# Performance work log

Measured on AMD Instinct MI355X. Metric: run time of the kernel, lower is better.

Reference implementation:

```python
import jax, jax.numpy as jnp
import numpy as np

NUM_HEADS = 12
NUM_GROUPS = 4
LN_EPS = 1e-12
NEG = -10000.0


def _ln(x, g, b):
    m = x.mean(-1, keepdims=True)
    v = ((x - m) ** 2).mean(-1, keepdims=True)
    return (x - m) * jax.lax.rsqrt(v + LN_EPS) * g + b


def _attention(h, ext_mask, Wattn, battn, ln):
    # h: [B,S,H]; ext_mask additive [B,1,1,S]; Wattn [4,H,H] = (q,k,v,o); battn [4,H]; ln [2,H]
    B, S, H = h.shape
    dh = H // NUM_HEADS
    q = (h @ Wattn[0] + battn[0]).reshape(B, S, NUM_HEADS, dh)
    k = (h @ Wattn[1] + battn[1]).reshape(B, S, NUM_HEADS, dh)
    v = (h @ Wattn[2] + battn[2]).reshape(B, S, NUM_HEADS, dh)
    scores = jnp.einsum('bqhd,bkhd->bhqk', q, k) * (1.0 / np.sqrt(dh)) + ext_mask
    p = jax.nn.softmax(scores, axis=-1)
    ctx = jnp.einsum('bhqk,bkhd->bqhd', p, v).reshape(B, S, H)
    # BertSelfOutput: dense + residual + LayerNorm
    return _ln(ctx @ Wattn[3] + battn[3] + h, ln[0], ln[1])


def _ffn(x, Wi, bi, Wo, bo, ln):
    # BertIntermediate (gelu) + BertOutput (dense + residual + LayerNorm)
    return _ln(jax.nn.gelu(x @ Wi + bi, approximate=False) @ Wo + bo + x, ln[0], ln[1])


def _bert_layer(h, ext_mask, Wattn, battn, ln_attn, Wi, bi, Wo, bo, ln_out):
    a = _attention(h, ext_mask, Wattn, battn, ln_attn)
    return _ffn(a, Wi, bi, Wo, bo, ln_out)


def _hier_attention(h, hier_mask, Wattn, battn, ln_attn, Wi, bi, Wo, bo, ln_out):
    # group masks [G,B,S]: 1 where hier_mask == group_id (ids 1..G)
    gids = jnp.arange(1, NUM_GROUPS + 1)
    masks = (hier_mask[None] == gids[:, None, None]).astype(h.dtype)  # [G,B,S]
    ext = (1.0 - masks)[:, :, None, None, :] * NEG                    # [G,B,1,1,S]
    # one full BertLayer per group (vectorized over G instead of batch concat)
    outs = jax.vmap(lambda m: _bert_layer(h, m, Wattn, battn, ln_attn, Wi, bi, Wo, bo, ln_out))(ext)  # [G,B,S,H]
    return jnp.sum(outs * masks[..., None], axis=0)


def reference(hidden_states, attention_mask, main_Wattn, main_battn, main_ln_attn,
              main_Wi, main_bi, main_Wo, main_bo, main_ln_out,
              hier_Wattn, hier_battn, hier_ln_attn, hier_Wi, hier_bi, hier_Wo,
              hier_bo, hier_ln_out, hier_mask):
    attn_out = _attention(hidden_states, attention_mask, main_Wattn, main_battn, main_ln_attn)
    hier_out = _hier_attention(hidden_states, hier_mask, hier_Wattn, hier_battn,
                               hier_ln_attn, hier_Wi, hier_bi, hier_Wo, hier_bo, hier_ln_out)
    combined = attn_out + hier_out
    return _ffn(combined, main_Wi, main_bi, main_Wo, main_bo, main_ln_out)


def setup_inputs() -> dict:
    key = jax.random.key(0)
    ks = jax.random.split(key, 20)
    B, S, H, F = 8, 512, 768, 3072
    W = 0.02  # weight init scale

    def layer_params(k):
        kk = jax.random.split(k, 8)
        return dict(
            Wattn=jax.random.normal(kk[0], (4, H, H), jnp.float32) * W,
            battn=jax.random.normal(kk[1], (4, H), jnp.float32) * W,
            ln_attn=jnp.stack([1.0 + jax.random.normal(kk[2], (H,), jnp.float32) * W,
                               jax.random.normal(kk[3], (H,), jnp.float32) * W]),
            Wi=jax.random.normal(kk[4], (H, F), jnp.float32) * W,
            bi=jax.random.normal(kk[5], (F,), jnp.float32) * W,
            Wo=jax.random.normal(kk[6], (F, H), jnp.float32) * W,
            bo=jax.random.normal(kk[7], (H,), jnp.float32) * W,
            ln_out=jnp.stack([1.0 + jax.random.normal(kk[2], (H,), jnp.float32) * W,
                              jax.random.normal(kk[3], (H,), jnp.float32) * W]),
        )

    main = layer_params(ks[0])
    hier = layer_params(ks[1])
    inp = {
        'hidden_states': jax.random.normal(ks[2], (B, S, H), jnp.float32),
        'attention_mask': jnp.zeros((B, 1, 1, S), jnp.float32),
        'hier_mask': jax.random.randint(ks[3], (B, S), 0, 5).astype(jnp.int64),
    }
    for name, p in (('main', main), ('hier', hier)):
        for k2, v in p.items():
            inp[f'{name}_{k2}'] = v
    return inp
```

## Files before the change

kernel.cpp:

```cpp
#include <hip/hip_runtime.h>
#include <hip/hip_bf16.h>

#define DI __device__ __forceinline__

typedef __attribute__((ext_vector_type(4))) float  f32x4;
typedef __attribute__((ext_vector_type(8))) short  s16x8;
typedef __attribute__((ext_vector_type(4))) short  s16x4;
typedef __attribute__((ext_vector_type(8))) __bf16 bf16x8;

DI short f2bf(float f) {
  union { float f; unsigned u; } v; v.f = f;
  unsigned r = v.u + 0x7fffu + ((v.u >> 16) & 1u);
  return (short)(r >> 16);
}

DI f32x4 mfma16(s16x8 a, s16x8 b, f32x4 c) {
  return __builtin_amdgcn_mfma_f32_16x16x32_bf16(
      __builtin_bit_cast(bf16x8, a), __builtin_bit_cast(bf16x8, b), c, 0, 0, 0);
}

typedef const __attribute__((address_space(1))) unsigned* gas_p;
typedef __attribute__((address_space(3))) unsigned* las_p;
DI void gload16(const void* g, void* l) {
  __builtin_amdgcn_global_load_lds((gas_p)g, (las_p)l, 16, 0, 0);
}

__global__ __launch_bounds__(256) void cast_bf16(const float* __restrict__ x,
                                                 short* __restrict__ y) {
  const int i = (blockIdx.x * 256 + threadIdx.x) * 4;
  const float4 t = *(const float4*)&x[i];
  s16x4 o;
  o[0] = f2bf(t.x); o[1] = f2bf(t.y); o[2] = f2bf(t.z); o[3] = f2bf(t.w);
  *(s16x4*)&y[i] = o;
}

struct TJob { const float* src; short* dst; int K, N, tile0; };
struct TJobs { TJob j[12]; };

__global__ __launch_bounds__(256) void transpose_w(TJobs jobs) {
  __shared__ float T[32][33];
  const int t = blockIdx.x;
  int ji = 0;
#pragma unroll
  for (int i = 1; i < 12; ++i) if (jobs.j[i].tile0 <= t) ji = i;
  const float* src = jobs.j[ji].src;
  short* dst = jobs.j[ji].dst;
  const int K = jobs.j[ji].K, N = jobs.j[ji].N;
  const int lt = t - jobs.j[ji].tile0;
  const int tn = N >> 5;
  const int n0 = (lt % tn) << 5, k0 = (lt / tn) << 5;
  const int tid = threadIdx.x;
#pragma unroll
  for (int i = 0; i < 4; ++i) {
    const int c = i * 256 + tid, r = c >> 5, cc = c & 31;
    T[cc][r] = src[(long long)(k0 + r) * N + n0 + cc];
  }
  __syncthreads();
#pragma unroll
  for (int i = 0; i < 4; ++i) {
    const int c = i * 256 + tid, r = c >> 5, cc = c & 31;
    dst[(long long)(n0 + r) * K + k0 + cc] = f2bf(T[r][cc]);
  }
}

__global__ __launch_bounds__(256) void transpose_v(const short* __restrict__ QKV,
                                                   short* __restrict__ Vt) {
  __shared__ short T[64][72];
  const int bh = blockIdx.y;
  const int b = bh / 12, hh = bh % 12;
  const int s0 = blockIdx.x * 64;
  const int tid = threadIdx.x;
#pragma unroll
  for (int i = 0; i < 2; ++i) {
    const int c = i * 256 + tid;
    const int s = c >> 3, d = (c & 7) * 8;
    s16x8 v = *(const s16x8*)&QKV[(long long)(b * 512 + s0 + s) * 2304 + 1536 + hh * 64 + d];
    *(s16x8*)&T[s][d] = v;
  }
  __syncthreads();
#pragma unroll
  for (int i = 0; i < 2; ++i) {
    const int c = i * 256 + tid;
    const int d = c >> 3, s = (c & 7) * 8;
    s16x8 v;
#pragma unroll
    for (int j = 0; j < 8; ++j) v[j] = T[s + j][d];
    *(s16x8*)&Vt[(long long)bh * 32768 + (long long)d * 512 + s0 + s] = v;
  }
}

template<int BM, int BN, int WM, int WN, int EPI>
__global__ __launch_bounds__(256) void gemm_bt(
    const short* __restrict__ A, int lda, long long sA,
    const short* __restrict__ B, int ldb, long long sB,
    void* __restrict__ Cv, int ldc,
    long long cOuter, int cInner, int cStride,
    const float* __restrict__ bias,
    int K, int nSplit) {
  constexpr int BK = 32;
  constexpr int WNW = BN / WN;
  constexpr int MFR = WM / 16, NFR = WN / 16;
  constexpr int ACH = BM * 4;
  constexpr int BCH = BN * 4;

  __shared__ short As[2][BM * BK];
  __shared__ short Bs[2][BN * BK];

  const int z = blockIdx.z;
  const int zb = z / nSplit, zs = z - zb * nSplit;
  const short* Ab = A + (long long)zb * sA + (long long)zs * K;
  const short* Bb = B + (long long)zb * sB + (long long)zs * K;
  const long long cOff = (long long)(z / cInner) * cOuter + (long long)(z % cInner) * cStride;

  const int bm = blockIdx.x * BM;
  const int bn = blockIdx.y * BN;
  const int tid = threadIdx.x;
  const int wave = tid >> 6, lane = tid & 63;
  const int wm = (wave / WNW) * WM;
  const int wn = (wave % WNW) * WN;
  const int l16 = lane & 15, lk = lane >> 4;

  f32x4 acc[MFR][NFR] = {};

  auto stage = [&](int buf, int kt) {
#pragma unroll
    for (int i = 0; i < ACH / 256; ++i) {
      const int c = i * 256 + tid;
      gload16(Ab + (long long)(bm + (c >> 2)) * lda + kt + (c & 3) * 8,
              &As[buf][(i * 256 + wave * 64) * 8]);
    }
#pragma unroll
    for (int i = 0; i < BCH / 256; ++i) {
      const int c = i * 256 + tid;
      gload16(Bb + (long long)(bn + (c >> 2)) * ldb + kt + (c & 3) * 8,
              &Bs[buf][(i * 256 + wave * 64) * 8]);
    }
  };

  stage(0, 0);
  __syncthreads();
  int cur = 0;
  for (int kt = 0; kt < K; kt += BK) {
    if (kt + BK < K) stage(cur ^ 1, kt + BK);
    s16x8 af[MFR], bfr[NFR];
#pragma unroll
    for (int mi = 0; mi < MFR; ++mi)
      af[mi] = *(const s16x8*)&As[cur][(wm + mi * 16 + l16) * BK + lk * 8];
#pragma unroll
    for (int ni = 0; ni < NFR; ++ni)
      bfr[ni] = *(const s16x8*)&Bs[cur][(wn + ni * 16 + l16) * BK + lk * 8];
#pragma unroll
    for (int mi = 0; mi < MFR; ++mi)
#pragma unroll
      for (int ni = 0; ni < NFR; ++ni)
        acc[mi][ni] = mfma16(bfr[ni], af[mi], acc[mi][ni]);
    __syncthreads();
    cur ^= 1;
  }

#pragma unroll
  for (int mi = 0; mi < MFR; ++mi) {
    const int row = bm + wm + mi * 16 + l16;
#pragma unroll
    for (int ni = 0; ni < NFR; ++ni) {
      const int col = bn + wn + ni * 16 + lk * 4;
      const long long idx = cOff + (long long)row * ldc + col;
      f32x4 bv = {};
      if (EPI != 2 && bias) bv = *(const f32x4*)&bias[col];
      f32x4 v = acc[mi][ni] + bv;
      if constexpr (EPI == 0) {
        s16x4 o;
#pragma unroll
        for (int r = 0; r < 4; ++r) o[r] = f2bf(v[r]);
        *(s16x4*)&((short*)Cv)[idx] = o;
      } else if constexpr (EPI == 1) {
        s16x4 o;
#pragma unroll
        for (int r = 0; r < 4; ++r) {
          const float g = 0.5f * v[r] * (1.f + erff(v[r] * 0.70710678118654752f));
          o[r] = f2bf(g);
        }
        *(s16x4*)&((short*)Cv)[idx] = o;
      } else {
        *(f32x4*)&((float*)Cv)[idx] = v;
      }
    }
  }
}

template<int HIER>
__global__ __launch_bounds__(256) void attn_scores(
    const short* __restrict__ QKV,
    const float* __restrict__ amask,
    const int* __restrict__ hmask,
    short* __restrict__ P) {
  __shared__ short Qs[32 * 64];
  __shared__ short Ks[256 * 64];
  __shared__ float red[32 * 4];
  __shared__ int   hm[512];

  const int bh = blockIdx.y;
  const int b = bh / 12, hh = bh % 12;
  const int q0 = blockIdx.x * 32;
  const int tid = threadIdx.x;
  const int wave = tid >> 6, lane = tid & 63;
  const int l16 = lane & 15, lk = lane >> 4;
  const long long rowbase = (long long)(b * 512) * 2304 + hh * 64;

  {
    const int c = tid;
    gload16(QKV + rowbase + (long long)(q0 + (c >> 3)) * 2304 + (c & 7) * 8,
            &Qs[wave * 64 * 8]);
  }
  if constexpr (HIER) {
    for (int i = tid; i < 512; i += 256) hm[i] = hmask[b * 512 + i];
  }

  f32x4 acc[2][8] = {};
#pragma unroll
  for (int kc = 0; kc < 2; ++kc) {
    if (kc) __syncthreads();
#pragma unroll
    for (int i = 0; i < 8; ++i) {
      const int c = i * 256 + tid;
      gload16(QKV + rowbase + 768 + (long long)(kc * 256 + (c >> 3)) * 2304 + (c & 7) * 8,
              &Ks[(i * 256 + wave * 64) * 8]);
    }
    __syncthreads();
#pragma unroll
    for (int ks = 0; ks < 2; ++ks) {
      s16x8 af[2], bfr[4];
#pragma unroll
      for (int mi = 0; mi < 2; ++mi)
        af[mi] = *(const s16x8*)&Qs[(mi * 16 + l16) * 64 + ks * 32 + lk * 8];
#pragma unroll
      for (int ni = 0; ni < 4; ++ni)
        bfr[ni] = *(const s16x8*)&Ks[(wave * 64 + ni * 16 + l16) * 64 + ks * 32 + lk * 8];
#pragma unroll
      for (int mi = 0; mi < 2; ++mi)
#pragma unroll
        for (int ni = 0; ni < 4; ++ni)
          acc[mi][kc * 4 + ni] = mfma16(af[mi], bfr[ni], acc[mi][kc * 4 + ni]);
    }
  }

  int gq[2][4];
  if constexpr (HIER) {
#pragma unroll
    for (int mi = 0; mi < 2; ++mi)
#pragma unroll
      for (int r = 0; r < 4; ++r)
        gq[mi][r] = hm[q0 + mi * 16 + lk * 4 + r];
  }
  int hk[8]; float am[8];
#pragma unroll
  for (int nig = 0; nig < 8; ++nig) {
    const int col = (nig >> 2) * 256 + wave * 64 + (nig & 3) * 16 + l16;
    if constexpr (HIER) hk[nig] = hm[col];
    else                am[nig] = amask[b * 512 + col];
  }
#pragma unroll
  for (int mi = 0; mi < 2; ++mi)
#pragma unroll
    for (int nig = 0; nig < 8; ++nig)
#pragma unroll
      for (int r = 0; r < 4; ++r) {
        float v = acc[mi][nig][r] * 0.125f;
        if constexpr (HIER) v += (hk[nig] == gq[mi][r]) ? 0.f : -10000.f;
        else                v += am[nig];
        acc[mi][nig][r] = v;
      }

  float mx[2][4];
#pragma unroll
  for (int mi = 0; mi < 2; ++mi)
#pragma unroll
    for (int r = 0; r < 4; ++r) {
      float m = acc[mi][0][r];
#pragma unroll
      for (int nig = 1; nig < 8; ++nig) m = fmaxf(m, acc[mi][nig][r]);
#pragma unroll
      for (int d = 1; d < 16; d <<= 1) m = fmaxf(m, __shfl_xor(m, d));
      mx[mi][r] = m;
      red[(mi * 16 + lk * 4 + r) * 4 + wave] = m;
    }
  __syncthreads();
#pragma unroll
  for (int mi = 0; mi < 2; ++mi)
#pragma unroll
    for (int r = 0; r < 4; ++r) {
      const int q = mi * 16 + lk * 4 + r;
      mx[mi][r] = fmaxf(fmaxf(red[q * 4], red[q * 4 + 1]),
                        fmaxf(red[q * 4 + 2], red[q * 4 + 3]));
    }
  __syncthreads();

  float sm[2][4];
#pragma unroll
  for (int mi = 0; mi < 2; ++mi)
#pragma unroll
    for (int r = 0; r < 4; ++r) {
      float s = 0.f;
#pragma unroll
      for (int nig = 0; nig < 8; ++nig) {
        const float e = __expf(acc[mi][nig][r] - mx[mi][r]);
        acc[mi][nig][r] = e;
        s += e;
      }
#pragma unroll
      for (int d = 1; d < 16; d <<= 1) s += __shfl_xor(s, d);
      sm[mi][r] = s;
      red[(mi * 16 + lk * 4 + r) * 4 + wave] = s;
    }
  __syncthreads();
#pragma unroll
  for (int mi = 0; mi < 2; ++mi)
#pragma unroll
    for (int r = 0; r < 4; ++r) {
      const int q = mi * 16 + lk * 4 + r;
      sm[mi][r] = 1.f / (red[q * 4] + red[q * 4 + 1] + red[q * 4 + 2] + red[q * 4 + 3]);
    }

  const long long Pbase = (long long)bh * 512 * 512;
#pragma unroll
  for (int mi = 0; mi < 2; ++mi)
#pragma unroll
    for (int nig = 0; nig < 8; ++nig) {
      const int col = (nig >> 2) * 256 + wave * 64 + (nig & 3) * 16 + l16;
#pragma unroll
      for (int r = 0; r < 4; ++r) {
        const int q = mi * 16 + lk * 4 + r;
        P[Pbase + (long long)(q0 + q) * 512 + col] = f2bf(acc[mi][nig][r] * sm[mi][r]);
      }
    }
}

template<int NS, int MODE>
__global__ __launch_bounds__(256) void ln_red(
    const float* __restrict__ part, const float* __restrict__ bias,
    const float* __restrict__ res, const float* __restrict__ ln,
    float* __restrict__ outf, short* __restrict__ outb,
    const int* __restrict__ hmask) {
  constexpr long long SP = 4096LL * 768;
  const int row = blockIdx.x * 4 + (threadIdx.x >> 6);
  const int lane = threadIdx.x & 63;
  const long long rb = (long long)row * 768;
  float v[12];
  float s = 0.f;
#pragma unroll
  for (int i = 0; i < 3; ++i) {
    const int c4 = lane + (i << 6);
    float4 t = ((const float4*)(res + rb))[c4];
    const float4 bv = ((const float4*)bias)[c4];
    t.x += bv.x; t.y += bv.y; t.z += bv.z; t.w += bv.w;
#pragma unroll
    for (int ss = 0; ss < NS; ++ss) {
      const float4 p = ((const float4*)(part + ss * SP + rb))[c4];
      t.x += p.x; t.y += p.y; t.z += p.z; t.w += p.w;
    }
    v[i * 4 + 0] = t.x; v[i * 4 + 1] = t.y; v[i * 4 + 2] = t.z; v[i * 4 + 3] = t.w;
    s += t.x + t.y + t.z + t.w;
  }
#pragma unroll
  for (int d = 1; d < 64; d <<= 1) s += __shfl_xor(s, d);
  const float mean = s * (1.f / 768.f);
  float vs = 0.f;
#pragma unroll
  for (int i = 0; i < 12; ++i) { const float dv = v[i] - mean; vs += dv * dv; }
#pragma unroll
  for (int d = 1; d < 64; d <<= 1) vs += __shfl_xor(vs, d);
  const float rstd = rsqrtf(vs * (1.f / 768.f) + 1e-12f);
  int keep = 1;
  if constexpr (MODE == 2) keep = (hmask[row] != 0);
#pragma unroll
  for (int i = 0; i < 3; ++i) {
    const int c4 = lane + (i << 6);
    const float4 g = ((const float4*)ln)[c4];
    const float4 be = ((const float4*)(ln + 768))[c4];
    const float gg[4] = {g.x, g.y, g.z, g.w}, bb[4] = {be.x, be.y, be.z, be.w};
    float resv[4];
#pragma unroll
    for (int j = 0; j < 4; ++j) {
      float yv = (v[i * 4 + j] - mean) * rstd * gg[j] + bb[j];
      if constexpr (MODE == 2) {
        const float a = outf[rb + c4 * 4 + j];
        yv = a + (keep ? yv : 0.f);
      }
      resv[j] = yv;
    }
    float4 of; of.x = resv[0]; of.y = resv[1]; of.z = resv[2]; of.w = resv[3];
    ((float4*)(outf + rb))[c4] = of;
    if constexpr (MODE >= 1) {
      s16x4 ob;
#pragma unroll
      for (int j = 0; j < 4; ++j) ob[j] = f2bf(resv[j]);
      *(s16x4*)&outb[rb + c4 * 4] = ob;
    }
  }
}

extern "C" void kernel_launch(void* const* d_in, const int* in_sizes, int n_in,
                              void* d_out, int out_size, void* d_ws, size_t ws_size,
                              hipStream_t stream) {
  (void)in_sizes; (void)n_in; (void)out_size; (void)ws_size;
  const float* h      = (const float*)d_in[0];
  const float* amask  = (const float*)d_in[1];
  const int*   hmask  = (const int*)d_in[2];
  const float* mWattn = (const float*)d_in[3];
  const float* mbattn = (const float*)d_in[4];
  const float* mlnA   = (const float*)d_in[5];
  const float* mWi    = (const float*)d_in[6];
  const float* mbi    = (const float*)d_in[7];
  const float* mWo    = (const float*)d_in[8];
  const float* mbo    = (const float*)d_in[9];
  const float* mlnO   = (const float*)d_in[10];
  const float* hWattn = (const float*)d_in[11];
  const float* hbattn = (const float*)d_in[12];
  const float* hlnA   = (const float*)d_in[13];
  const float* hWi    = (const float*)d_in[14];
  const float* hbi    = (const float*)d_in[15];
  const float* hWo    = (const float*)d_in[16];
  const float* hbo    = (const float*)d_in[17];
  const float* hlnO   = (const float*)d_in[18];
  float* out = (float*)d_out;

  char* ws = (char*)d_ws;
  size_t off = 0;
  auto alloc = [&](size_t bytes) {
    void* p = ws + off;
    off += (bytes + 255) & ~(size_t)255;
    return p;
  };
  short* wq_m = (short*)alloc(2304ull * 768 * 2);
  short* wq_h = (short*)alloc(2304ull * 768 * 2);
  short* wo2  = (short*)alloc(2ull * 768 * 768 * 2);
  short* wi_m = (short*)alloc(3072ull * 768 * 2);
  short* wi_h = (short*)alloc(3072ull * 768 * 2);
  short* wf_m = (short*)alloc(768ull * 3072 * 2);
  short* wf_h = (short*)alloc(768ull * 3072 * 2);
  short* hbf  = (short*)alloc(4096ull * 768 * 2);
  short* qkv  = (short*)alloc(4096ull * 2304 * 2);
  short* vt   = (short*)alloc(96ull * 64 * 512 * 2);
  short* Pb   = (short*)alloc(96ull * 512 * 512 * 2);
  short* ctxb = (short*)alloc(2ull * 4096 * 768 * 2);
  float* pre1 = (float*)alloc(4096ull * 768 * 4);
  float* attn = (float*)alloc(4096ull * 768 * 4);
  short* abf  = (short*)alloc(4096ull * 768 * 2);
  short* cbf  = (short*)alloc(4096ull * 768 * 2);
  short* mid  = qkv;
  float* part = (float*)Pb;

  const long long SC = 4096LL * 768;

  cast_bf16<<<dim3(3072), dim3(256), 0, stream>>>(h, hbf);

  TJobs tj; int tile = 0; int nj = 0;
  auto add = [&](const float* s, short* d, int K, int N) {
    tj.j[nj].src = s; tj.j[nj].dst = d; tj.j[nj].K = K; tj.j[nj].N = N; tj.j[nj].tile0 = tile;
    tile += (K / 32) * (N / 32); nj++;
  };
  add(mWattn,              wq_m,              768, 768);
  add(mWattn + 589824,     wq_m + 589824,     768, 768);
  add(mWattn + 2 * 589824, wq_m + 2 * 589824, 768, 768);
  add(mWattn + 3 * 589824, wo2,               768, 768);
  add(mWi,                 wi_m,              768, 3072);
  add(mWo,                 wf_m,              3072, 768);
  add(hWattn,              wq_h,              768, 768);
  add(hWattn + 589824,     wq_h + 589824,     768, 768);
  add(hWattn + 2 * 589824, wq_h + 2 * 589824, 768, 768);
  add(hWattn + 3 * 589824, wo2 + 589824,      768, 768);
  add(hWi,                 wi_h,              768, 3072);
  add(hWo,                 wf_h,              3072, 768);
  transpose_w<<<dim3(tile), dim3(256), 0, stream>>>(tj);

  auto attn_path = [&](const short* wq, const float* battn, int hier, short* ctx) {
    gemm_bt<128, 128, 64, 64, 0><<<dim3(32, 18, 1), dim3(256), 0, stream>>>(
        hbf, 768, 0, wq, 768, 0, qkv, 2304, 0, 1, 0, battn, 768, 1);
    transpose_v<<<dim3(8, 96), dim3(256), 0, stream>>>(qkv, vt);
    if (hier)
      attn_scores<1><<<dim3(16, 96), dim3(256), 0, stream>>>(qkv, amask, hmask, Pb);
    else
      attn_scores<0><<<dim3(16, 96), dim3(256), 0, stream>>>(qkv, amask, hmask, Pb);
    gemm_bt<128, 64, 32, 64, 0><<<dim3(4, 1, 96), dim3(256), 0, stream>>>(
        Pb, 512, 262144LL, vt, 512, 32768LL,
        ctx, 768, 512LL * 768, 12, 64, nullptr, 512, 1);
  };

  attn_path(wq_m, mbattn, 0, ctxb);
  attn_path(wq_h, hbattn, 1, ctxb + SC);

  gemm_bt<128, 128, 64, 64, 2><<<dim3(32, 6, 4), dim3(256), 0, stream>>>(
      ctxb, 768, SC, wo2, 768, 589824LL, part, 768, SC, 1, 0, nullptr, 384, 2);
  ln_red<2, 0><<<dim3(1024), dim3(256), 0, stream>>>(
      part, mbattn + 2304, h, mlnA, attn, nullptr, nullptr);
  ln_red<2, 1><<<dim3(1024), dim3(256), 0, stream>>>(
      part + 2 * SC, hbattn + 2304, h, hlnA, pre1, abf, nullptr);

  gemm_bt<128, 128, 64, 64, 1><<<dim3(32, 24, 1), dim3(256), 0, stream>>>(
      abf, 768, 0, wi_h, 768, 0, mid, 3072, 0, 1, 0, hbi, 768, 1);
  gemm_bt<128, 128, 64, 64, 2><<<dim3(32, 6, 4), dim3(256), 0, stream>>>(
      mid, 3072, 0, wf_h, 3072, 0, part, 768, SC, 1, 0, nullptr, 768, 4);
  ln_red<4, 2><<<dim3(1024), dim3(256), 0, stream>>>(
      part, hbo, pre1, hlnO, attn, cbf, hmask);

  gemm_bt<128, 128, 64, 64, 1><<<dim3(32, 24, 1), dim3(256), 0, stream>>>(
      cbf, 768, 0, wi_m, 768, 0, mid, 3072, 0, 1, 0, mbi, 768, 1);
  gemm_bt<128, 128, 64, 64, 2><<<dim3(32, 6, 4), dim3(256), 0, stream>>>(
      mid, 3072, 0, wf_m, 3072, 0, part, 768, SC, 1, 0, nullptr, 768, 4);
  ln_red<4, 0><<<dim3(1024), dim3(256), 0, stream>>>(
      part, mbo, attn, mlnO, out, nullptr, nullptr);
}
```

Measured before the change: 379.6 us.

## Triple-buffer GEMM LDS staging with vmcnt waits and single barrier

Moves the bf16 GEMM from double-buffered LDS to a three-stage ring. It prefetches two K-tiles ahead and waits on outstanding loads with explicit s_waitcnt vmcnt, using one s_barrier per iteration instead of two __syncthreads. The staging address math is hoisted into per-thread base pointers. The intent is deeper overlap of global-to-LDS loads with MFMA work and less barrier overhead, at the cost of 1.5x LDS use, which may lower occupancy. There is also a correctness risk: the tile written two iterations ahead may overlap buffers other waves are still reading.

Result: no change. 384.5 us (+1.3%).

```diff
diff --git a/kernel.cpp b/kernel.cpp
--- a/kernel.cpp
+++ b/kernel.cpp
@@ -23,6 +23,10 @@
 typedef __attribute__((address_space(3))) unsigned* las_p;
 DI void gload16(const void* g, void* l) {
   __builtin_amdgcn_global_load_lds((gas_p)g, (las_p)l, 16, 0, 0);
+}
+
+template<int N> DI void wait_vmcnt() {
+  asm volatile("s_waitcnt vmcnt(%0)" :: "n"(N) : "memory");
 }
 
 __global__ __launch_bounds__(256) void cast_bf16(const float* __restrict__ x,
@@ -100,11 +104,12 @@
   constexpr int BK = 32;
   constexpr int WNW = BN / WN;
   constexpr int MFR = WM / 16, NFR = WN / 16;
-  constexpr int ACH = BM * 4;
-  constexpr int BCH = BN * 4;
-
-  __shared__ short As[2][BM * BK];
-  __shared__ short Bs[2][BN * BK];
+  constexpr int ALD = BM / 64;
+  constexpr int BLD = BN / 64;
+  constexpr int LPT = ALD + BLD;
+
+  __shared__ short As[3][BM * BK];
+  __shared__ short Bs[3][BN * BK];
 
   const int z = blockIdx.z;
   const int zb = z / nSplit, zs = z - zb * nSplit;
@@ -120,28 +125,29 @@
   const int wn = (wave % WNW) * WN;
   const int l16 = lane & 15, lk = lane >> 4;
 
+  const short* aBase = Ab + (long long)(bm + (tid >> 2)) * lda + (tid & 3) * 8;
+  const short* bBase = Bb + (long long)(bn + (tid >> 2)) * ldb + (tid & 3) * 8;
+  const int ldsOff = wave * 64 * 8;
+
   f32x4 acc[MFR][NFR] = {};
 
   auto stage = [&](int buf, int kt) {
 #pragma unroll
-    for (int i = 0; i < ACH / 256; ++i) {
-      const int c = i * 256 + tid;
-      gload16(Ab + (long long)(bm + (c >> 2)) * lda + kt + (c & 3) * 8,
-              &As[buf][(i * 256 + wave * 64) * 8]);
-    }
-#pragma unroll
-    for (int i = 0; i < BCH / 256; ++i) {
-      const int c = i * 256 + tid;
-      gload16(Bb + (long long)(bn + (c >> 2)) * ldb + kt + (c & 3) * 8,
-              &Bs[buf][(i * 256 + wave * 64) * 8]);
-    }
+    for (int i = 0; i < ALD; ++i)
+      gload16(aBase + kt + (long long)(i * 64) * lda, &As[buf][i * 2048 + ldsOff]);
+#pragma unroll
+    for (int i = 0; i < BLD; ++i)
+      gload16(bBase + kt + (long long)(i * 64) * ldb, &Bs[buf][i * 2048 + ldsOff]);
   };
 
+  const int nt = K / BK;
   stage(0, 0);
-  __syncthreads();
+  if (nt > 1) stage(1, BK);
   int cur = 0;
-  for (int kt = 0; kt < K; kt += BK) {
-    if (kt + BK < K) stage(cur ^ 1, kt + BK);
+  for (int t = 0; t < nt; ++t) {
+    if (t + 1 < nt) wait_vmcnt<LPT>();
+    else            wait_vmcnt<0>();
+    __builtin_amdgcn_s_barrier();
     s16x8 af[MFR], bfr[NFR];
 #pragma unroll
     for (int mi = 0; mi < MFR; ++mi)
@@ -154,8 +160,11 @@
 #pragma unroll
       for (int ni = 0; ni < NFR; ++ni)
         acc[mi][ni] = mfma16(bfr[ni], af[mi], acc[mi][ni]);
-    __syncthreads();
-    cur ^= 1;
+    if (t + 2 < nt) {
+      const int nb = cur + 2 >= 3 ? cur - 1 : cur + 2;
+      stage(nb, (t + 2) * BK);
+    }
+    cur = (cur + 1 == 3) ? 0 : cur + 1;
   }
 
 #pragma unroll
```
